# Kernel tuning notes

Hardware: AMD Instinct MI355X
Metric: run time of the kernel (lower is better)

Reference implementation:

```python
import jax, jax.numpy as jnp
import numpy as np

WS = 7    # window size
SS = 3    # shift size
NH = 6    # num heads
EPS = 1e-5


def _ln(x, g, b):
    m = jnp.mean(x, -1, keepdims=True)
    v = jnp.mean((x - m) ** 2, -1, keepdims=True)
    return (x - m) * jax.lax.rsqrt(v + EPS) * g + b


def _win_part(x, ws):
    # (B, H, W, C) -> (B*nW, ws*ws, C)
    B, H, W, C = x.shape
    x = x.reshape(B, H // ws, ws, W // ws, ws, C).transpose(0, 1, 3, 2, 4, 5)
    return x.reshape(-1, ws * ws, C)


def _win_rev(w, ws, B, H, W):
    # (B*nW, ws*ws, C) -> (B, H, W, C)
    C = w.shape[-1]
    x = w.reshape(B, H // ws, W // ws, ws, ws, C).transpose(0, 1, 3, 2, 4, 5)
    return x.reshape(B, H, W, C)


def _forward(x, norm1_g, norm1_b, qkv_w, qkv_b, proj_w, proj_b, norm2_g, norm2_b,
             fc1_w, fc1_b, fc2_w, fc2_b, rel_table, mask_matrix, H, W, rel_index):
    B, L, C = x.shape
    hd = C // NH
    shortcut = x
    h = _ln(x, norm1_g, norm1_b).reshape(B, H, W, C)
    pad_r = (WS - W % WS) % WS
    pad_b = (WS - H % WS) % WS
    h = jnp.pad(h, ((0, 0), (0, pad_b), (0, pad_r), (0, 0)))
    Hp, Wp = H + pad_b, W + pad_r
    # cyclic shift (shift_size > 0 path)
    h = jnp.roll(h, (-SS, -SS), axis=(1, 2))
    xw = _win_part(h, WS)                                   # [Bw, N, C]
    Bw, N, _ = xw.shape
    qkv = (xw @ qkv_w + qkv_b).reshape(Bw, N, 3, NH, hd)
    q = qkv[:, :, 0].transpose(0, 2, 1, 3) * (hd ** -0.5)   # [Bw, NH, N, hd]
    k = qkv[:, :, 1].transpose(0, 2, 1, 3)
    v = qkv[:, :, 2].transpose(0, 2, 1, 3)
    attn = q @ k.transpose(0, 1, 3, 2)                      # [Bw, NH, N, N]
    bias = rel_table[rel_index.reshape(-1)].reshape(N, N, NH).transpose(2, 0, 1)
    attn = attn + bias[None]
    nW = mask_matrix.shape[0]
    attn = attn.reshape(Bw // nW, nW, NH, N, N) + mask_matrix[None, :, None]
    attn = jax.nn.softmax(attn.reshape(Bw, NH, N, N), axis=-1)
    o = (attn @ v).transpose(0, 2, 1, 3).reshape(Bw, N, C)
    o = o @ proj_w + proj_b
    h = _win_rev(o, WS, B, Hp, Wp)
    h = jnp.roll(h, (SS, SS), axis=(1, 2))[:, :H, :W, :].reshape(B, L, C)
    x = shortcut + h
    y = _ln(x, norm2_g, norm2_b)
    y = jax.nn.gelu(y @ fc1_w + fc1_b, approximate=False) @ fc2_w + fc2_b  # torch GELU = exact erf
    return x + y


def setup_inputs() -> dict:
    B, H, W, C, HID = 32, 56, 56, 192, 768
    ws, ss = WS, SS
    ks = jax.random.split(jax.random.key(0), 8)
    rn = lambda i, shp, s: jax.random.normal(ks[i], shp, jnp.float32) * s
    inp = {
        'x': rn(0, (B, H * W, C), 1.0),
        'norm1_g': jnp.ones((C,), jnp.float32), 'norm1_b': jnp.zeros((C,), jnp.float32),
        'qkv_w': rn(1, (C, 3 * C), 0.02), 'qkv_b': jnp.zeros((3 * C,), jnp.float32),
        'proj_w': rn(2, (C, C), 0.02), 'proj_b': jnp.zeros((C,), jnp.float32),
        'norm2_g': jnp.ones((C,), jnp.float32), 'norm2_b': jnp.zeros((C,), jnp.float32),
        'fc1_w': rn(3, (C, HID), 0.02), 'fc1_b': jnp.zeros((HID,), jnp.float32),
        'fc2_w': rn(4, (HID, C), 0.02), 'fc2_b': jnp.zeros((C,), jnp.float32),
        'rel_table': rn(5, ((2 * ws - 1) ** 2, NH), 0.02),
    }
    # relative position index (same construction as torch buffer)
    coords = np.stack(np.meshgrid(np.arange(ws), np.arange(ws), indexing='ij')).reshape(2, -1)
    rel = (coords[:, :, None] - coords[:, None, :]).transpose(1, 2, 0)
    rel[..., 0] += ws - 1
    rel[..., 1] += ws - 1
    rel[..., 0] *= 2 * ws - 1
    inp['rel_index'] = jnp.asarray(rel.sum(-1), jnp.int32)  # [49, 49]
    # shifted-window attention mask (standard Swin construction)
    img = np.zeros((1, H, W, 1), np.float32)
    cnt = 0
    for hs in (slice(0, -ws), slice(-ws, -ss), slice(-ss, None)):
        for wsl in (slice(0, -ws), slice(-ws, -ss), slice(-ss, None)):
            img[:, hs, wsl, :] = cnt
            cnt += 1
    mw = img.reshape(1, H // ws, ws, W // ws, ws, 1).transpose(0, 1, 3, 2, 4, 5).reshape(-1, ws * ws)
    diff = mw[:, None, :] - mw[:, :, None]
    inp['mask_matrix'] = jnp.asarray(np.where(diff != 0, -100.0, 0.0), jnp.float32)  # [64, 49, 49]
    inp['H'] = H
    inp['W'] = W
    return inp


def reference(x, norm1_g, norm1_b, qkv_w, qkv_b, proj_w, proj_b, norm2_g, norm2_b,
              fc1_w, fc1_b, fc2_w, fc2_b, rel_table, rel_index, mask_matrix, H, W):
    return _forward(x, norm1_g, norm1_b, qkv_w, qkv_b, proj_w, proj_b, norm2_g, norm2_b,
                    fc1_w, fc1_b, fc2_w, fc2_b, rel_table, mask_matrix, H, W, rel_index)
```

## Files before the change

kernel.cpp:

```cpp
#include <hip/hip_runtime.h>

typedef __bf16 bf8 __attribute__((ext_vector_type(8)));
typedef float f4 __attribute__((ext_vector_type(4)));

__device__ __forceinline__ float b2f(unsigned short u) {
  union { unsigned int i; float f; } c; c.i = ((unsigned int)u) << 16; return c.f;
}
__device__ __forceinline__ unsigned short f2b(float f) {
  union { float f; unsigned int i; } c; c.f = f;
  unsigned int i = c.i;
  return (unsigned short)((i + 0x7FFFu + ((i >> 16) & 1u)) >> 16);
}

__device__ __forceinline__ void gl_lds16(const unsigned short* g, unsigned short* l) {
  __builtin_amdgcn_global_load_lds((const __attribute__((address_space(1))) unsigned int*)g,
                                   (__attribute__((address_space(3))) unsigned int*)l,
                                   16, 0, 0);
}

__device__ __forceinline__ float gelu_fast(float v) {
  float w = v * v;
  float u = v * (-1.59576912f - 0.07135481f * w);
  return v / (1.0f + __expf(u));
}

__global__ void transpose_kernel(const float* __restrict__ in,
                                 unsigned short* __restrict__ out, int K, int N) {
  int idx = blockIdx.x * 256 + threadIdx.x;
  if (idx < K * N) {
    int n = idx / K, k = idx - n * K;
    out[idx] = f2b(in[k * N + n]);
  }
}

__global__ __launch_bounds__(256) void ln_kernel(const float* __restrict__ xin,
                                                 const float* __restrict__ g,
                                                 const float* __restrict__ bb,
                                                 unsigned short* __restrict__ out) {
  long token = (long)blockIdx.x * 4 + (threadIdx.x >> 6);
  int lane = threadIdx.x & 63;
  const float* row = xin + token * 192;
  float v[3] = {row[lane], row[lane + 64], row[lane + 128]};
  float s = v[0] + v[1] + v[2];
#pragma unroll
  for (int m = 1; m < 64; m <<= 1) s += __shfl_xor(s, m, 64);
  float mean = s * (1.0f / 192.0f);
  float d0 = v[0] - mean, d1 = v[1] - mean, d2 = v[2] - mean;
  float dd = d0 * d0 + d1 * d1 + d2 * d2;
#pragma unroll
  for (int m = 1; m < 64; m <<= 1) dd += __shfl_xor(dd, m, 64);
  float rstd = rsqrtf(dd * (1.0f / 192.0f) + 1e-5f);
  unsigned short* orow = out + token * 192;
#pragma unroll
  for (int i = 0; i < 3; i++) {
    int c = lane + i * 64;
    orow[c] = f2b((v[i] - mean) * rstd * g[c] + bb[c]);
  }
}

template <int EPI>
__global__ __launch_bounds__(256) void gemm_kernel(const unsigned short* __restrict__ A,
                                                   const unsigned short* __restrict__ Bt,
                                                   const float* __restrict__ bias,
                                                   const float* __restrict__ res,
                                                   void* __restrict__ out, int K, int N) {
  __shared__ __align__(16) unsigned short As[2][128 * 64];
  __shared__ __align__(16) unsigned short Bs[2][64 * 64];
  const int tid = threadIdx.x;
  const int wave = tid >> 6;
  const int lane = tid & 63;
  const int quad = lane >> 4;
  const int l16 = lane & 15;

  const int NX = gridDim.x;
  int lin = blockIdx.y * NX + blockIdx.x;
  const int T = NX * gridDim.y;
  if ((T & 7) == 0) {
    lin = (lin & 7) * (T >> 3) + (lin >> 3);
  }
  const int bx = lin % NX;
  const int by = lin / NX;
  const long m0 = (long)by * 128;
  const long n0 = (long)bx * 64;

  long a_src[4];
  int a_dstc[4];
#pragma unroll
  for (int j = 0; j < 4; ++j) {
    int L = (wave * 4 + j) * 64 + lane;
    int row = L >> 3, cs = L & 7;
    a_src[j] = (m0 + row) * (long)K + ((cs ^ (row & 7)) << 3);
    a_dstc[j] = (wave * 4 + j) * 512;
  }
  long b_src[2];
  int b_dstc[2];
#pragma unroll
  for (int j = 0; j < 2; ++j) {
    int L = (wave * 2 + j) * 64 + lane;
    int row = L >> 3, cs = L & 7;
    b_src[j] = (n0 + row) * (long)K + ((cs ^ (row & 7)) << 3);
    b_dstc[j] = (wave * 2 + j) * 512;
  }

  const int nT = K >> 6;
  f4 acc[2][4] = {};

#pragma unroll
  for (int j = 0; j < 4; ++j) gl_lds16(A + a_src[j], &As[0][a_dstc[j]]);
#pragma unroll
  for (int j = 0; j < 2; ++j) gl_lds16(Bt + b_src[j], &Bs[0][b_dstc[j]]);

  int cur = 0;
  for (int t = 0; t < nT; ++t) {
    if (t + 1 < nT) {
      const int k0 = (t + 1) << 6;
#pragma unroll
      for (int j = 0; j < 4; ++j) gl_lds16(A + a_src[j] + k0, &As[cur ^ 1][a_dstc[j]]);
#pragma unroll
      for (int j = 0; j < 2; ++j) gl_lds16(Bt + b_src[j] + k0, &Bs[cur ^ 1][b_dstc[j]]);
      asm volatile("s_waitcnt vmcnt(6)" ::: "memory");
    } else {
      asm volatile("s_waitcnt vmcnt(0)" ::: "memory");
    }
    __builtin_amdgcn_s_barrier();
    __builtin_amdgcn_sched_barrier(0);
#pragma unroll
    for (int kk = 0; kk < 2; ++kk) {
      bf8 a[2], b[4];
#pragma unroll
      for (int mt = 0; mt < 2; ++mt) {
        int r = wave * 32 + mt * 16 + l16;
        int c = kk * 4 + quad;
        a[mt] = *(const bf8*)&As[cur][r * 64 + ((c ^ (r & 7)) << 3)];
      }
#pragma unroll
      for (int nt = 0; nt < 4; ++nt) {
        int r = nt * 16 + l16;
        int c = kk * 4 + quad;
        b[nt] = *(const bf8*)&Bs[cur][r * 64 + ((c ^ (r & 7)) << 3)];
      }
#pragma unroll
      for (int mt = 0; mt < 2; ++mt)
#pragma unroll
        for (int nt = 0; nt < 4; ++nt)
          acc[mt][nt] = __builtin_amdgcn_mfma_f32_16x16x32_bf16(a[mt], b[nt], acc[mt][nt], 0, 0, 0);
    }
    __builtin_amdgcn_sched_barrier(0);
    __builtin_amdgcn_s_barrier();
    cur ^= 1;
  }

#pragma unroll
  for (int nt = 0; nt < 4; ++nt) {
    long n = n0 + nt * 16 + l16;
    float bv = bias[n];
#pragma unroll
    for (int mt = 0; mt < 2; ++mt) {
#pragma unroll
      for (int r = 0; r < 4; ++r) {
        long m = m0 + wave * 32 + mt * 16 + quad * 4 + r;
        float v = acc[mt][nt][r] + bv;
        long idx = m * N + n;
        if (EPI == 0) {
          ((unsigned short*)out)[idx] = f2b(v);
        } else if (EPI == 1) {
          ((float*)out)[idx] = v + res[idx];
        } else if (EPI == 2) {
          ((unsigned short*)out)[idx] = f2b(gelu_fast(v));
        } else {
          ((float*)out)[idx] = v + res[idx];
        }
      }
    }
  }
}

__global__ __launch_bounds__(128) void attn_kernel(const unsigned short* __restrict__ qkv,
                                                   const float* __restrict__ rel_t,
                                                   unsigned short* __restrict__ o) {
  __shared__ __align__(16) unsigned short sh[2 * 6912];
  __shared__ float relh[2][170];
  __shared__ int toksh[2][49];
  __shared__ int zsh[2][49];
  const int wave = threadIdx.x >> 6;
  const int lane = threadIdx.x & 63;
  const int quad = lane >> 4;
  const int l16 = lane & 15;
  const int p = blockIdx.x * 2 + wave;
  const int head = p % 6;
  const int wib = p / 6;
  const int wi = wib & 63;
  const int b = wib >> 6;
  unsigned short* Vts = sh + wave * 6912;
  unsigned short* Ps = Vts + 2304;

  if (lane < 49) {
    int r = lane / 7, c = lane - (lane / 7) * 7;
    int ph = (wi >> 3) * 7 + r, pw = (wi & 7) * 7 + c;
    int h = ph + 3; if (h >= 56) h -= 56;
    int w = pw + 3; if (w >= 56) w -= 56;
    toksh[wave][lane] = (b * 56 + h) * 56 + w;
    int zh = (ph < 49) ? 0 : (ph < 53 ? 1 : 2);
    int zw = (pw < 49) ? 0 : (pw < 53 ? 1 : 2);
    zsh[wave][lane] = zh * 3 + zw;
  }
  for (int i = lane; i < 169; i += 64) relh[wave][i] = rel_t[i * 6 + head];
  {
#pragma unroll
    for (int e = 0; e < 4; e++) {
      int ee = lane + e * 64;
      int d = ee >> 3, c8 = ee & 7;
      *(unsigned int*)&Vts[d * 72 + 48 + c8 * 2] = 0u;
    }
  }
  __syncthreads();

  for (int e = lane; e < 196; e += 64) {
    int n = e >> 2, c = e & 3;
    int t = toksh[wave][n];
    uint4 vc = *(const uint4*)(qkv + (long)t * 576 + head * 32 + 384 + c * 8);
    const unsigned short* vv = (const unsigned short*)&vc;
#pragma unroll
    for (int j = 0; j < 8; j++) Vts[(c * 8 + j) * 72 + n] = vv[j];
  }

  bf8 zv;
#pragma unroll
  for (int q8 = 0; q8 < 8; q8++) zv[q8] = (__bf16)0.0f;
  bf8 af[4], bf_[4];
#pragma unroll
  for (int i = 0; i < 4; i++) {
    int row = 16 * i + l16;
    int rv = row < 49 ? row : 48;
    long base = (long)toksh[wave][rv] * 576 + head * 32 + quad * 8;
    bf8 qf = *(const bf8*)(qkv + base);
    bf8 kf = *(const bf8*)(qkv + base + 192);
    if (row >= 49) { qf = zv; kf = zv; }
    af[i] = qf;
    bf_[i] = kf;
  }

  f4 S[4][4];
#pragma unroll
  for (int i = 0; i < 4; i++)
#pragma unroll
    for (int j = 0; j < 4; j++)
      S[i][j] = __builtin_amdgcn_mfma_f32_16x16x32_bf16(af[i], bf_[j], (f4){0.f, 0.f, 0.f, 0.f}, 0, 0, 0);

  int colv[4], colkey[4], zcol[4];
#pragma unroll
  for (int jt = 0; jt < 4; jt++) {
    int col = 16 * jt + l16;
    int cc = col < 49 ? col : 48;
    int rj = cc / 7, cj = cc - rj * 7;
    colkey[jt] = rj * 13 + cj;
    zcol[jt] = zsh[wave][cc];
    colv[jt] = (col < 49);
  }

  __syncthreads();

  const float sc = 0.17677669529663687f;
#pragma unroll
  for (int it = 0; it < 4; it++) {
#pragma unroll
    for (int r = 0; r < 4; r++) {
      int row = 16 * it + quad * 4 + r;
      int row2 = row < 49 ? row : 48;
      int ri = row2 / 7, ci = row2 - ri * 7;
      int rk = ri * 13 + ci + 84;
      int zr = zsh[wave][row2];
      float v[4];
#pragma unroll
      for (int jt = 0; jt < 4; jt++) {
        float bias = relh[wave][rk - colkey[jt]];
        float msk = (zr == zcol[jt]) ? 0.0f : -100.0f;
        float val = S[it][jt][r] * sc + bias + msk;
        v[jt] = colv[jt] ? val : -1e30f;
      }
      float mx = fmaxf(fmaxf(v[0], v[1]), fmaxf(v[2], v[3]));
#pragma unroll
      for (int m = 1; m < 16; m <<= 1) mx = fmaxf(mx, __shfl_xor(mx, m, 64));
      float e0 = __expf(v[0] - mx), e1 = __expf(v[1] - mx), e2 = __expf(v[2] - mx), e3 = __expf(v[3] - mx);
      float sum = e0 + e1 + e2 + e3;
#pragma unroll
      for (int m = 1; m < 16; m <<= 1) sum += __shfl_xor(sum, m, 64);
      float inv = 1.0f / sum;
      Ps[row * 72 + 0 + l16] = f2b(e0 * inv);
      Ps[row * 72 + 16 + l16] = f2b(e1 * inv);
      Ps[row * 72 + 32 + l16] = f2b(e2 * inv);
      Ps[row * 72 + 48 + l16] = f2b(e3 * inv);
    }
  }
  __syncthreads();

  f4 O[4][2] = {};
#pragma unroll
  for (int ks = 0; ks < 2; ks++) {
    bf8 pv[2];
#pragma unroll
    for (int nt = 0; nt < 2; nt++) pv[nt] = *(const bf8*)&Vts[(16 * nt + l16) * 72 + ks * 32 + quad * 8];
#pragma unroll
    for (int mt = 0; mt < 4; mt++) {
      bf8 pa = *(const bf8*)&Ps[(16 * mt + l16) * 72 + ks * 32 + quad * 8];
#pragma unroll
      for (int nt = 0; nt < 2; nt++)
        O[mt][nt] = __builtin_amdgcn_mfma_f32_16x16x32_bf16(pa, pv[nt], O[mt][nt], 0, 0, 0);
    }
  }
#pragma unroll
  for (int mt = 0; mt < 4; mt++) {
#pragma unroll
    for (int r = 0; r < 4; r++) {
      int row = 16 * mt + quad * 4 + r;
      if (row < 49) {
        long base = (long)toksh[wave][row] * 192 + head * 32 + l16;
        o[base] = f2b(O[mt][0][r]);
        o[base + 16] = f2b(O[mt][1][r]);
      }
    }
  }
}

extern "C" void kernel_launch(void* const* d_in, const int* in_sizes, int n_in,
                              void* d_out, int out_size, void* d_ws, size_t ws_size,
                              hipStream_t stream) {
  const float* x      = (const float*)d_in[0];
  const float* n1g    = (const float*)d_in[1];
  const float* n1b    = (const float*)d_in[2];
  const float* qkv_w  = (const float*)d_in[3];
  const float* qkv_b  = (const float*)d_in[4];
  const float* proj_w = (const float*)d_in[5];
  const float* proj_b = (const float*)d_in[6];
  const float* n2g    = (const float*)d_in[7];
  const float* n2b    = (const float*)d_in[8];
  const float* fc1_w  = (const float*)d_in[9];
  const float* fc1_b  = (const float*)d_in[10];
  const float* fc2_w  = (const float*)d_in[11];
  const float* fc2_b  = (const float*)d_in[12];
  const float* rel_t  = (const float*)d_in[13];
  const float* mask   = (const float*)d_in[15];
  (void)mask;

  char* ws = (char*)d_ws;
  unsigned short* qkv_wT  = (unsigned short*)(ws + 0);
  unsigned short* proj_wT = (unsigned short*)(ws + 221184);
  unsigned short* fc1_wT  = (unsigned short*)(ws + 294912);
  unsigned short* fc2_wT  = (unsigned short*)(ws + 589824);
  unsigned short* bufA    = (unsigned short*)(ws + 884736);
  unsigned short* bufB    = (unsigned short*)(ws + 39419904ULL);
  float*          xres    = (float*)(ws + 193560576ULL);

  const int M = 100352;

  transpose_kernel<<<(192 * 576 + 255) / 256, 256, 0, stream>>>(qkv_w, qkv_wT, 192, 576);
  transpose_kernel<<<(192 * 192 + 255) / 256, 256, 0, stream>>>(proj_w, proj_wT, 192, 192);
  transpose_kernel<<<(192 * 768 + 255) / 256, 256, 0, stream>>>(fc1_w, fc1_wT, 192, 768);
  transpose_kernel<<<(768 * 192 + 255) / 256, 256, 0, stream>>>(fc2_w, fc2_wT, 768, 192);

  ln_kernel<<<M / 4, 256, 0, stream>>>(x, n1g, n1b, bufA);
  gemm_kernel<0><<<dim3(576 / 64, M / 128), 256, 0, stream>>>(bufA, qkv_wT, qkv_b, nullptr, bufB, 192, 576);
  attn_kernel<<<12288 / 2, 128, 0, stream>>>(bufB, rel_t, bufA);
  gemm_kernel<1><<<dim3(192 / 64, M / 128), 256, 0, stream>>>(bufA, proj_wT, proj_b, x, xres, 192, 192);
  ln_kernel<<<M / 4, 256, 0, stream>>>(xres, n2g, n2b, bufA);
  gemm_kernel<2><<<dim3(768 / 64, M / 128), 256, 0, stream>>>(bufA, fc1_wT, fc1_b, nullptr, bufB, 192, 768);
  gemm_kernel<3><<<dim3(192 / 64, M / 128), 256, 0, stream>>>(bufB, fc2_wT, fc2_b, xres, d_out, 768, 192);
}
```

Before: 506.4 us.

## Fuse projection GEMM with residual add and second LayerNorm; use native bf16 stores

Adds a proj_ln_kernel in which each block computes all 192 output columns of the projection GEMM for 128 rows. It then adds bias and the residual, writes the fp32 residual stream, and applies LayerNorm2 in registers to write the bf16 normalized output. This removes the separate LayerNorm pass over the fp32 residual buffer and one kernel launch. Separately, the manual rounding helper f2b is replaced by a native __bf16 cast for all bf16 stores. The fused kernel uses 80KB of LDS and 96 accumulator registers per thread, which limits occupancy, and it writes its output in place over its own input buffer rows.

```diff
diff --git a/kernel.cpp b/kernel.cpp
--- a/kernel.cpp
+++ b/kernel.cpp
@@ -3,14 +3,7 @@
 typedef __bf16 bf8 __attribute__((ext_vector_type(8)));
 typedef float f4 __attribute__((ext_vector_type(4)));
 
-__device__ __forceinline__ float b2f(unsigned short u) {
-  union { unsigned int i; float f; } c; c.i = ((unsigned int)u) << 16; return c.f;
-}
-__device__ __forceinline__ unsigned short f2b(float f) {
-  union { float f; unsigned int i; } c; c.f = f;
-  unsigned int i = c.i;
-  return (unsigned short)((i + 0x7FFFu + ((i >> 16) & 1u)) >> 16);
-}
+__device__ __forceinline__ void stb(unsigned short* p, float v) { *(__bf16*)p = (__bf16)v; }
 
 __device__ __forceinline__ void gl_lds16(const unsigned short* g, unsigned short* l) {
   __builtin_amdgcn_global_load_lds((const __attribute__((address_space(1))) unsigned int*)g,
@@ -29,7 +22,7 @@
   int idx = blockIdx.x * 256 + threadIdx.x;
   if (idx < K * N) {
     int n = idx / K, k = idx - n * K;
-    out[idx] = f2b(in[k * N + n]);
+    stb(&out[idx], in[k * N + n]);
   }
 }
 
@@ -54,7 +47,7 @@
 #pragma unroll
   for (int i = 0; i < 3; i++) {
     int c = lane + i * 64;
-    orow[c] = f2b((v[i] - mean) * rstd * g[c] + bb[c]);
+    stb(&orow[c], (v[i] - mean) * rstd * g[c] + bb[c]);
   }
 }
 
@@ -162,14 +155,136 @@
         float v = acc[mt][nt][r] + bv;
         long idx = m * N + n;
         if (EPI == 0) {
-          ((unsigned short*)out)[idx] = f2b(v);
-        } else if (EPI == 1) {
-          ((float*)out)[idx] = v + res[idx];
+          stb(&((unsigned short*)out)[idx], v);
         } else if (EPI == 2) {
-          ((unsigned short*)out)[idx] = f2b(gelu_fast(v));
+          stb(&((unsigned short*)out)[idx], gelu_fast(v));
         } else {
           ((float*)out)[idx] = v + res[idx];
         }
+      }
+    }
+  }
+}
+
+__global__ __launch_bounds__(256) void proj_ln_kernel(const unsigned short* __restrict__ A,
+                                                      const unsigned short* __restrict__ Bt,
+                                                      const float* __restrict__ bias,
+                                                      const float* __restrict__ res,
+                                                      const float* __restrict__ g2,
+                                                      const float* __restrict__ b2,
+                                                      float* __restrict__ xres,
+                                                      unsigned short* __restrict__ lnout) {
+  __shared__ __align__(16) unsigned short As[2][128 * 64];
+  __shared__ __align__(16) unsigned short Bs[2][192 * 64];
+  const int tid = threadIdx.x;
+  const int wave = tid >> 6;
+  const int lane = tid & 63;
+  const int quad = lane >> 4;
+  const int l16 = lane & 15;
+
+  int lin = blockIdx.y;
+  const int T = gridDim.y;
+  if ((T & 7) == 0) lin = (lin & 7) * (T >> 3) + (lin >> 3);
+  const long m0 = (long)lin * 128;
+
+  long a_src[4];
+  int a_dstc[4];
+#pragma unroll
+  for (int j = 0; j < 4; ++j) {
+    int L = (wave * 4 + j) * 64 + lane;
+    int row = L >> 3, cs = L & 7;
+    a_src[j] = (m0 + row) * 192L + ((cs ^ (row & 7)) << 3);
+    a_dstc[j] = (wave * 4 + j) * 512;
+  }
+  long b_src[6];
+  int b_dstc[6];
+#pragma unroll
+  for (int j = 0; j < 6; ++j) {
+    int L = (wave * 6 + j) * 64 + lane;
+    int row = L >> 3, cs = L & 7;
+    b_src[j] = row * 192L + ((cs ^ (row & 7)) << 3);
+    b_dstc[j] = (wave * 6 + j) * 512;
+  }
+
+  f4 acc[2][12] = {};
+
+#pragma unroll
+  for (int j = 0; j < 4; ++j) gl_lds16(A + a_src[j], &As[0][a_dstc[j]]);
+#pragma unroll
+  for (int j = 0; j < 6; ++j) gl_lds16(Bt + b_src[j], &Bs[0][b_dstc[j]]);
+
+  int cur = 0;
+  for (int t = 0; t < 3; ++t) {
+    if (t + 1 < 3) {
+      const int k0 = (t + 1) << 6;
+#pragma unroll
+      for (int j = 0; j < 4; ++j) gl_lds16(A + a_src[j] + k0, &As[cur ^ 1][a_dstc[j]]);
+#pragma unroll
+      for (int j = 0; j < 6; ++j) gl_lds16(Bt + b_src[j] + k0, &Bs[cur ^ 1][b_dstc[j]]);
+      asm volatile("s_waitcnt vmcnt(10)" ::: "memory");
+    } else {
+      asm volatile("s_waitcnt vmcnt(0)" ::: "memory");
+    }
+    __builtin_amdgcn_s_barrier();
+    __builtin_amdgcn_sched_barrier(0);
+#pragma unroll
+    for (int kk = 0; kk < 2; ++kk) {
+      bf8 a[2];
+#pragma unroll
+      for (int mt = 0; mt < 2; ++mt) {
+        int r = wave * 32 + mt * 16 + l16;
+        int c = kk * 4 + quad;
+        a[mt] = *(const bf8*)&As[cur][r * 64 + ((c ^ (r & 7)) << 3)];
+      }
+#pragma unroll
+      for (int nt = 0; nt < 12; ++nt) {
+        int r = nt * 16 + l16;
+        int c = kk * 4 + quad;
+        bf8 b = *(const bf8*)&Bs[cur][r * 64 + ((c ^ (r & 7)) << 3)];
+#pragma unroll
+        for (int mt = 0; mt < 2; ++mt)
+          acc[mt][nt] = __builtin_amdgcn_mfma_f32_16x16x32_bf16(a[mt], b, acc[mt][nt], 0, 0, 0);
+      }
+    }
+    __builtin_amdgcn_sched_barrier(0);
+    __builtin_amdgcn_s_barrier();
+    cur ^= 1;
+  }
+
+#pragma unroll
+  for (int mt = 0; mt < 2; ++mt) {
+#pragma unroll
+    for (int r = 0; r < 4; ++r) {
+      long mm = m0 + wave * 32 + mt * 16 + quad * 4 + r;
+      const float* rrow = res + mm * 192;
+      float v[12];
+      float s = 0.0f;
+#pragma unroll
+      for (int nt = 0; nt < 12; ++nt) {
+        int n = nt * 16 + l16;
+        float t = acc[mt][nt][r] + bias[n] + rrow[n];
+        v[nt] = t;
+        s += t;
+      }
+#pragma unroll
+      for (int m = 1; m < 16; m <<= 1) s += __shfl_xor(s, m, 64);
+      float mean = s * (1.0f / 192.0f);
+      float d = 0.0f;
+#pragma unroll
+      for (int nt = 0; nt < 12; ++nt) {
+        float dd = v[nt] - mean;
+        d += dd * dd;
+      }
+#pragma unroll
+      for (int m = 1; m < 16; m <<= 1) d += __shfl_xor(d, m, 64);
+      float rstd = rsqrtf(d * (1.0f / 192.0f) + 1e-5f);
+      float* xrow = xres + mm * 192;
+      unsigned short* lrow = lnout + mm * 192;
+#pragma unroll
+      for (int nt = 0; nt < 12; ++nt) {
+        int n = nt * 16 + l16;
+        xrow[n] = v[nt];
+        stb(&lrow[n], (v[nt] - mean) * rstd * g2[n] + b2[n]);
       }
     }
   }
@@ -286,10 +401,10 @@
 #pragma unroll
       for (int m = 1; m < 16; m <<= 1) sum += __shfl_xor(sum, m, 64);
       float inv = 1.0f / sum;
-      Ps[row * 72 + 0 + l16] = f2b(e0 * inv);
-      Ps[row * 72 + 16 + l16] = f2b(e1 * inv);
-      Ps[row * 72 + 32 + l16] = f2b(e2 * inv);
-      Ps[row * 72 + 48 + l16] = f2b(e3 * inv);
+      stb(&Ps[row * 72 + 0 + l16], e0 * inv);
+      stb(&Ps[row * 72 + 16 + l16], e1 * inv);
+      stb(&Ps[row * 72 + 32 + l16], e2 * inv);
+      stb(&Ps[row * 72 + 48 + l16], e3 * inv);
     }
   }
   __syncthreads();
@@ -315,8 +430,8 @@
       int row = 16 * mt + quad * 4 + r;
       if (row < 49) {
         long base = (long)toksh[wave][row] * 192 + head * 32 + l16;
-        o[base] = f2b(O[mt][0][r]);
-        o[base + 16] = f2b(O[mt][1][r]);
+        stb(&o[base], O[mt][0][r]);
+        stb(&o[base + 16], O[mt][1][r]);
       }
     }
   }
@@ -361,8 +476,7 @@
   ln_kernel<<<M / 4, 256, 0, stream>>>(x, n1g, n1b, bufA);
   gemm_kernel<0><<<dim3(576 / 64, M / 128), 256, 0, stream>>>(bufA, qkv_wT, qkv_b, nullptr, bufB, 192, 576);
   attn_kernel<<<12288 / 2, 128, 0, stream>>>(bufB, rel_t, bufA);
-  gemm_kernel<1><<<dim3(192 / 64, M / 128), 256, 0, stream>>>(bufA, proj_wT, proj_b, x, xres, 192, 192);
-  ln_kernel<<<M / 4, 256, 0, stream>>>(xres, n2g, n2b, bufA);
+  proj_ln_kernel<<<dim3(1, M / 128), 256, 0, stream>>>(bufA, proj_wT, proj_b, x, n2g, n2b, xres, bufA);
   gemm_kernel<2><<<dim3(768 / 64, M / 128), 256, 0, stream>>>(bufA, fc1_wT, fc1_b, nullptr, bufB, 192, 768);
   gemm_kernel<3><<<dim3(192 / 64, M / 128), 256, 0, stream>>>(bufB, fc2_wT, fc2_b, xres, d_out, 768, 192);
 }
```

Measured after the change: 504.6 us. Within noise of the previous version (-0.3%).
